# Optimization experiments

Hardware: AMD Instinct MI355X
Metric: run time of the kernel (lower is better)

## Reference

```python
import jax, jax.numpy as jnp
import numpy as np

H = 16          # num_heads (init kwarg)
EPS = 1e-6      # LayerNorm eps


def rope_freqs(L, d):
    # interleaved RoPE freqs, repeat(f, 'i j -> i (j r)', r=2)
    t = jnp.arange(L, dtype=jnp.float32)
    inv = 1.0 / (10000.0 ** (jnp.arange(0, d, 2, dtype=jnp.float32) / d))
    f = t[:, None] * inv[None, :]          # (L, d//2)
    return jnp.repeat(f, 2, axis=-1)       # (L, d)


def rotate_half(x):
    # pair adjacent elems: (x1, x2) -> (-x2, x1)
    shp = x.shape
    x = x.reshape(shp[:-1] + (shp[-1] // 2, 2))
    x1, x2 = x[..., 0], x[..., 1]
    return jnp.stack((-x2, x1), axis=-1).reshape(shp)


def apply_rope(x, f):
    # x: (B, H, L, d), f: (L, d)
    return x * jnp.cos(f) + rotate_half(x) * jnp.sin(f)


def layernorm(x, g, b):
    m = jnp.mean(x, axis=-1, keepdims=True)
    v = jnp.mean(jnp.square(x - m), axis=-1, keepdims=True)
    return (x - m) * jax.lax.rsqrt(v + EPS) * g + b


def setup_inputs() -> dict:
    key = jax.random.key(0)
    ks = jax.random.split(key, 12)
    B, L, D = 2, 2048, 1024
    Dff = 4 * D
    s = 0.02
    inp = {
        'x': jax.random.normal(ks[0], (B, L, D), jnp.float32),
        'ln1_g': jnp.ones((D,), jnp.float32),
        'ln1_b': jnp.zeros((D,), jnp.float32),
        'wq': jax.random.normal(ks[1], (D, D), jnp.float32) * s,
        'bq': jnp.zeros((D,), jnp.float32),
        'wk': jax.random.normal(ks[2], (D, D), jnp.float32) * s,
        'bk': jnp.zeros((D,), jnp.float32),
        'wv': jax.random.normal(ks[3], (D, D), jnp.float32) * s,
        'bv': jnp.zeros((D,), jnp.float32),
        'wo': jax.random.normal(ks[4], (D, D), jnp.float32) * s,
        'bo': jnp.zeros((D,), jnp.float32),
        'ln2_g': jnp.ones((D,), jnp.float32),
        'ln2_b': jnp.zeros((D,), jnp.float32),
        'w1': jax.random.normal(ks[5], (D, Dff), jnp.float32) * s,
        'b1': jnp.zeros((Dff,), jnp.float32),
        'w2': jax.random.normal(ks[6], (Dff, D), jnp.float32) * s,
        'b2': jnp.zeros((D,), jnp.float32),
        # gates are zero-init in the module; use small random so the block is exercised
        'gate_msa': jax.random.normal(ks[7], (1, 1, D), jnp.float32) * 0.1,
        'gate_mlp': jax.random.normal(ks[8], (1, 1, D), jnp.float32) * 0.1,
    }
    return inp


def reference(x, ln1_g, ln1_b, wq, bq, wk, bk, wv, bv, wo, bo,
              ln2_g, ln2_b, w1, b1, w2, b2, gate_msa, gate_mlp):
    B, L, D = x.shape
    hd = D // H
    # --- self-attention branch ---
    h = layernorm(x, ln1_g, ln1_b)
    q = (h @ wq + bq).reshape(B, L, H, hd).transpose(0, 2, 1, 3)  # (B,H,L,hd)
    k = (h @ wk + bk).reshape(B, L, H, hd).transpose(0, 2, 1, 3)
    v = (h @ wv + bv).reshape(B, L, H, hd).transpose(0, 2, 1, 3)
    f = rope_freqs(L, hd)
    q = apply_rope(q, f)
    k = apply_rope(k, f)
    scores = jnp.einsum('bhic,bhjc->bhij', q, k) / np.float32(np.sqrt(hd))
    attn = jax.nn.softmax(scores, axis=-1)  # dropout disabled (eval)
    o = jnp.einsum('bhij,bhjc->bhic', attn, v)
    o = o.transpose(0, 2, 1, 3).reshape(B, L, D)
    x = x + gate_msa * (o @ wo + bo)
    # --- gated MLP branch ---
    h2 = layernorm(x, ln2_g, ln2_b)
    mlp = jax.nn.gelu(h2 @ w1 + b1, approximate=False) @ w2 + b2
    return x + gate_mlp * mlp
```

## Files before the change

kernel.cpp:

```cpp
#include <hip/hip_runtime.h>

typedef unsigned short u16;
typedef __attribute__((ext_vector_type(4))) float f32x4;
typedef __attribute__((ext_vector_type(8))) short bf16x8;

#define DEV static __device__ __forceinline__

DEV float bf2f(u16 u) { unsigned int i = ((unsigned int)u) << 16; return __builtin_bit_cast(float, i); }
DEV u16 f2bf(float f) {
  unsigned int x = __builtin_bit_cast(unsigned int, f);
  x += 0x7fffu + ((x >> 16) & 1u);
  return (u16)(x >> 16);
}

DEV unsigned cvtpk(float lo, float hi) {
  unsigned r;
  asm("v_cvt_pk_bf16_f32 %0, %1, %2" : "=v"(r) : "v"(lo), "v"(hi));
  return r;
}
DEV float exp2a(float x) {
  float r;
  asm("v_exp_f32 %0, %1" : "=v"(r) : "v"(x));
  return r;
}

template <int N>
DEV void wait_vmcnt() {
  if constexpr (N == 0) asm volatile("s_waitcnt vmcnt(0)" ::: "memory");
  else if constexpr (N == 3) asm volatile("s_waitcnt vmcnt(3)" ::: "memory");
  else if constexpr (N == 4) asm volatile("s_waitcnt vmcnt(4)" ::: "memory");
  else static_assert(N == 0, "unsupported vmcnt");
}

DEV void gload16(const u16* g, u16* l) {
  __builtin_amdgcn_global_load_lds(
      (const __attribute__((address_space(1))) unsigned int*)g,
      (__attribute__((address_space(3))) unsigned int*)l, 16, 0, 0);
}

__global__ __launch_bounds__(256) void ln_k(const float* __restrict__ x,
                                            const float* __restrict__ g,
                                            const float* __restrict__ b,
                                            u16* __restrict__ out) {
  const int row = blockIdx.x;
  const int t = threadIdx.x;
  const float4 v = *(const float4*)(x + (size_t)row * 1024 + t * 4);
  float s = v.x + v.y + v.z + v.w;
  float q = v.x * v.x + v.y * v.y + v.z * v.z + v.w * v.w;
#pragma unroll
  for (int m = 1; m < 64; m <<= 1) { s += __shfl_xor(s, m); q += __shfl_xor(q, m); }
  __shared__ float ss[4], qs[4];
  if ((t & 63) == 0) { ss[t >> 6] = s; qs[t >> 6] = q; }
  __syncthreads();
  s = ss[0] + ss[1] + ss[2] + ss[3];
  q = qs[0] + qs[1] + qs[2] + qs[3];
  const float mean = s * (1.0f / 1024.0f);
  const float var = q * (1.0f / 1024.0f) - mean * mean;
  const float rs = rsqrtf(var + 1e-6f);
  const float4 gv = *(const float4*)(g + t * 4);
  const float4 bv = *(const float4*)(b + t * 4);
  ushort4 o;
  o.x = f2bf((v.x - mean) * rs * gv.x + bv.x);
  o.y = f2bf((v.y - mean) * rs * gv.y + bv.y);
  o.z = f2bf((v.z - mean) * rs * gv.z + bv.z);
  o.w = f2bf((v.w - mean) * rs * gv.w + bv.w);
  *(ushort4*)(out + (size_t)row * 1024 + t * 4) = o;
}

__global__ __launch_bounds__(256) void tcvt_k(const float* __restrict__ src,
                                              u16* __restrict__ dst, int K, int N) {
  __shared__ u16 tl[32][33];
  const int k0 = blockIdx.x * 32, n0 = blockIdx.y * 32;
  const int c = threadIdx.x & 31, r0 = threadIdx.x >> 5;
#pragma unroll
  for (int p = 0; p < 4; p++) {
    const int r = p * 8 + r0;
    tl[r][c] = f2bf(src[(size_t)(k0 + r) * N + n0 + c]);
  }
  __syncthreads();
#pragma unroll
  for (int p = 0; p < 4; p++) {
    const int r = p * 8 + r0;
    dst[(size_t)(n0 + r) * K + k0 + c] = tl[c][r];
  }
}

template <int EPI, int TN>
__global__ __launch_bounds__(256) void gemm_bt(const u16* __restrict__ A,
                                               const u16* __restrict__ Bt,
                                               const float* __restrict__ bias,
                                               const float* __restrict__ resid,
                                               const float* __restrict__ gate,
                                               void* __restrict__ outv,
                                               int M, int N, int K) {
  constexpr int MI = (TN == 128) ? 4 : 2;
  constexpr int WRS = (TN == 128) ? 64 : 32;
  constexpr int L = 2 + TN / 64;
  __shared__ __align__(16) u16 lA[3][128 * 32];
  __shared__ __align__(16) u16 lB[3][TN * 32];
  const int tid = threadIdx.x;
  const int lane = tid & 63, wid = tid >> 6;
  const int l4 = lane >> 4, l15 = lane & 15;
  const int wr = (TN == 128) ? (wid >> 1) : wid;
  const int wc = (TN == 128) ? (wid & 1) : 0;
  const int mBase = blockIdx.x * 128;
  const int nBase = blockIdx.y * TN;

  f32x4 acc[MI][4];
#pragma unroll
  for (int i = 0; i < MI; i++)
#pragma unroll
    for (int j = 0; j < 4; j++)
#pragma unroll
      for (int e = 0; e < 4; e++) acc[i][j][e] = 0.f;

  const int sRow = tid >> 2;
  const int sCol = (((tid & 3) ^ ((sRow >> 1) & 3))) * 8;
  const int rsw = (l15 >> 1) & 3;

#define STAGE(bufi, k0)                                                               \
  {                                                                                   \
    _Pragma("unroll") for (int p = 0; p < 2; p++)                                     \
        gload16(A + (size_t)(mBase + p * 64 + sRow) * K + (k0) + sCol,                \
                &lA[bufi][p * 2048 + wid * 512]);                                     \
    _Pragma("unroll") for (int p = 0; p < TN / 64; p++)                               \
        gload16(Bt + (size_t)(nBase + p * 64 + sRow) * K + (k0) + sCol,               \
                &lB[bufi][p * 2048 + wid * 512]);                                     \
  }

  const int nt = K >> 5;
  STAGE(0, 0);
  STAGE(1, 32);
  wait_vmcnt<L>();
  __builtin_amdgcn_s_barrier();
  __builtin_amdgcn_sched_barrier(0);

  int bsel = 0;
  for (int it = 0; it < nt; ++it) {
    bf16x8 af[MI], bfr[4];
#pragma unroll
    for (int mi = 0; mi < MI; mi++)
      af[mi] = *(const bf16x8*)(&lA[bsel][(wr * WRS + mi * 16 + l15) * 32 + (l4 ^ rsw) * 8]);
#pragma unroll
    for (int ni = 0; ni < 4; ni++)
      bfr[ni] = *(const bf16x8*)(&lB[bsel][(wc * 64 + ni * 16 + l15) * 32 + (l4 ^ rsw) * 8]);
    if (it + 2 < nt) {
      int b2 = bsel + 2; if (b2 >= 3) b2 -= 3;
      STAGE(b2, (it + 2) * 32);
    }
#pragma unroll
    for (int mi = 0; mi < MI; mi++)
#pragma unroll
      for (int ni = 0; ni < 4; ni++)
        acc[mi][ni] = __builtin_amdgcn_mfma_f32_16x16x32_bf16(af[mi], bfr[ni], acc[mi][ni], 0, 0, 0);
    if (it + 1 < nt) {
      asm volatile("s_waitcnt lgkmcnt(0)" ::: "memory");
      __builtin_amdgcn_sched_barrier(0);
      if (it + 2 < nt) wait_vmcnt<L>();
      else wait_vmcnt<0>();
      __builtin_amdgcn_s_barrier();
      __builtin_amdgcn_sched_barrier(0);
    }
    bsel = (bsel == 2) ? 0 : bsel + 1;
  }
#undef STAGE

  u16* obf = (u16*)outv;
  float* of = (float*)outv;
#pragma unroll
  for (int mi = 0; mi < MI; mi++) {
#pragma unroll
    for (int ni = 0; ni < 4; ni++) {
      const int row0 = mBase + wr * WRS + mi * 16 + l4 * 4;
      const int col = nBase + wc * 64 + ni * 16 + l15;
      const float bb = bias[col];
#pragma unroll
      for (int r = 0; r < 4; r++) {
        const float v = acc[mi][ni][r] + bb;
        const size_t idx = (size_t)(row0 + r) * N + col;
        if (EPI == 0) {
          obf[idx] = f2bf(v);
        } else if (EPI == 1) {
          const float ge = 0.5f * v * (1.0f + erff(v * 0.70710678118654752f));
          obf[idx] = f2bf(ge);
        } else if (EPI == 2) {
          of[idx] = resid[idx] + gate[col] * v;
        } else {
          of[idx] = of[idx] + gate[col] * v;
        }
      }
    }
  }
}

__global__ __launch_bounds__(256) void rope_k(const u16* __restrict__ qkv,
                                              u16* __restrict__ qr, u16* __restrict__ kr) {
  const int sel = blockIdx.y;
  const int rid = blockIdx.x * 8 + (threadIdx.x >> 5);
  const int i = threadIdx.x & 31;
  const int b = rid >> 15;
  const int h = (rid >> 11) & 15;
  const int t = rid & 2047;
  const u16* src = qkv + (size_t)(b * 2048 + t) * 3072 + sel * 1024 + h * 64 + 2 * i;
  const ushort2 uv = *(const ushort2*)src;
  const float x0 = bf2f(uv.x), x1 = bf2f(uv.y);
  const float inv = __expf(-(float)i * 0.28782313662425572f);
  float sn, cs;
  sincosf((float)t * inv, &sn, &cs);
  const float sc = sel ? 1.0f : 0.18033688011112042f;
  ushort2 ov;
  ov.x = f2bf((x0 * cs - x1 * sn) * sc);
  ov.y = f2bf((x1 * cs + x0 * sn) * sc);
  *(ushort2*)((sel ? kr : qr) + (size_t)rid * 64 + 2 * i) = ov;
}

__global__ __launch_bounds__(256) void vtrans_k(const u16* __restrict__ qkv, u16* __restrict__ vt) {
  __shared__ u16 tl[64][65];
  const int bh = blockIdx.x >> 5;
  const int t0 = (blockIdx.x & 31) * 64;
  const int b = bh >> 4, h = bh & 15;
  const int tid = threadIdx.x;
#pragma unroll
  for (int p = 0; p < 16; p++) {
    const int e = p * 256 + tid;
    const int tr = e >> 6, d = e & 63;
    tl[tr][d] = qkv[(size_t)(b * 2048 + t0 + tr) * 3072 + 2048 + h * 64 + d];
  }
  __syncthreads();
#pragma unroll
  for (int p = 0; p < 16; p++) {
    const int e = p * 256 + tid;
    const int dr = e >> 6, tc = e & 63;
    vt[(size_t)(bh * 64 + dr) * 2048 + t0 + tc] = tl[tc][dr];
  }
}

__global__ __launch_bounds__(256) void attn_k(const u16* __restrict__ q,
                                              const u16* __restrict__ k,
                                              const u16* __restrict__ vt,
                                              u16* __restrict__ o) {
  const int bh = blockIdx.y;
  const int tid = threadIdx.x;
  const int wid = tid >> 6, lane = tid & 63;
  const int l4 = lane >> 4, l15 = lane & 15;
  const int qrow0 = blockIdx.x * 64 + wid * 16;

  __shared__ __align__(16) u16 kls[2][4096];
  __shared__ __align__(16) u16 vls[2][4096];
  __shared__ __align__(16) u16 pls[4][1024];

  const size_t qoff = ((size_t)bh * 2048 + qrow0) * 64;
  const bf16x8 qf0 = *(const bf16x8*)(q + qoff + (size_t)l15 * 64 + l4 * 8);
  const bf16x8 qf1 = *(const bf16x8*)(q + qoff + (size_t)l15 * 64 + 32 + l4 * 8);

  float m0 = -1e30f, ls0 = 0.f;
  f32x4 oacc[4];
#pragma unroll
  for (int ni = 0; ni < 4; ni++)
#pragma unroll
    for (int e = 0; e < 4; e++) oacc[ni][e] = 0.f;

  const char* kg = (const char*)(k + (size_t)bh * 2048 * 64);
  const char* vg = (const char*)(vt + (size_t)bh * 64 * 2048);
  const int sA = tid, sB = 256 + tid;
  const int rA = sA >> 3, cA = ((sA & 7) ^ (rA & 7)) << 4;
  const int rB = sB >> 3, cB = ((sB & 7) ^ (rB & 7)) << 4;
  u16* kd0 = &kls[0][(size_t)(wid * 64) * 8];
  u16* kd1 = &kls[0][(size_t)(256 + wid * 64) * 8];
  u16* vd0 = &vls[0][(size_t)(wid * 64) * 8];
  u16* vd1 = &vls[0][(size_t)(256 + wid * 64) * 8];

#define STAGE(bufi, kv0)                                                            \
  {                                                                                 \
    const int _o = (bufi)*4096;                                                     \
    gload16((const u16*)(kg + (size_t)((kv0) + rA) * 128 + cA), kd0 + _o);          \
    gload16((const u16*)(kg + (size_t)((kv0) + rB) * 128 + cB), kd1 + _o);          \
    gload16((const u16*)(vg + (size_t)rA * 4096 + (kv0)*2 + cA), vd0 + _o);         \
    gload16((const u16*)(vg + (size_t)rB * 4096 + (kv0)*2 + cB), vd1 + _o);         \
  }

  STAGE(0, 0);
  __syncthreads();

  char* P = (char*)pls[wid];
  char* prow0 = P + l15 * 128;
  const int psw = (l15 & 7) << 4;

  int buf = 0;
  for (int it = 0; it < 32; ++it) {
    if (it < 31) STAGE(buf ^ 1, (it + 1) * 64);
    const char* K = (const char*)kls[buf];
    const char* V = (const char*)vls[buf];

    f32x4 s0[4];
#pragma unroll
    for (int kt = 0; kt < 4; kt++) {
      const int row = kt * 16 + l15;
      const int sw = (row & 7) << 4;
      const char* kr = K + row * 128;
      const bf16x8 kf0 = *(const bf16x8*)(kr + ((l4 * 16) ^ sw));
      const bf16x8 kf1 = *(const bf16x8*)(kr + ((64 + l4 * 16) ^ sw));
      f32x4 z0 = {0.f, 0.f, 0.f, 0.f};
      z0 = __builtin_amdgcn_mfma_f32_16x16x32_bf16(kf0, qf0, z0, 0, 0, 0);
      s0[kt] = __builtin_amdgcn_mfma_f32_16x16x32_bf16(kf1, qf1, z0, 0, 0, 0);
    }

    float a00 = fmaxf(fmaxf(s0[0][0], s0[0][1]), fmaxf(s0[0][2], s0[0][3]));
    float a01 = fmaxf(fmaxf(s0[1][0], s0[1][1]), fmaxf(s0[1][2], s0[1][3]));
    float a02 = fmaxf(fmaxf(s0[2][0], s0[2][1]), fmaxf(s0[2][2], s0[2][3]));
    float a03 = fmaxf(fmaxf(s0[3][0], s0[3][1]), fmaxf(s0[3][2], s0[3][3]));
    float pm0 = fmaxf(fmaxf(a00, a01), fmaxf(a02, a03));
    pm0 = fmaxf(pm0, __shfl_xor(pm0, 16));
    pm0 = fmaxf(pm0, __shfl_xor(pm0, 32));
    const bool need = !__all(pm0 <= m0 + 11.54f);
    float al0 = 1.0f;
    if (need) {
      const float mn0 = fmaxf(m0, pm0);
      al0 = exp2a(m0 - mn0);
      m0 = mn0;
    }
#pragma unroll
    for (int kt = 0; kt < 4; kt++)
#pragma unroll
      for (int r = 0; r < 4; r++) s0[kt][r] = exp2a(s0[kt][r] - m0);
    float e00 = (s0[0][0] + s0[0][1]) + (s0[0][2] + s0[0][3]);
    float e01 = (s0[1][0] + s0[1][1]) + (s0[1][2] + s0[1][3]);
    float e02 = (s0[2][0] + s0[2][1]) + (s0[2][2] + s0[2][3]);
    float e03 = (s0[3][0] + s0[3][1]) + (s0[3][2] + s0[3][3]);
    float ps0 = (e00 + e01) + (e02 + e03);
    ps0 += __shfl_xor(ps0, 16);
    ps0 += __shfl_xor(ps0, 32);
    ls0 = ls0 * al0 + ps0;

#pragma unroll
    for (int kt = 0; kt < 4; kt++) {
      uint2 w0;
      w0.x = cvtpk(s0[kt][0], s0[kt][1]);
      w0.y = cvtpk(s0[kt][2], s0[kt][3]);
      *(uint2*)(prow0 + ((kt * 32 + l4 * 8) ^ psw)) = w0;
    }
    asm volatile("s_waitcnt lgkmcnt(0)" ::: "memory");
    const bf16x8 pa0 = *(const bf16x8*)(prow0 + ((l4 * 16) ^ psw));
    const bf16x8 pa1 = *(const bf16x8*)(prow0 + ((64 + l4 * 16) ^ psw));
    if (need) {
      f32x4 av;
#pragma unroll
      for (int r = 0; r < 4; r++) av[r] = __shfl(al0, l4 * 4 + r);
#pragma unroll
      for (int ni = 0; ni < 4; ni++) oacc[ni] *= av;
    }

#pragma unroll
    for (int ni = 0; ni < 4; ni++) {
      const int vrow = ni * 16 + l15;
      const int vsw = (vrow & 7) << 4;
      const char* vr = V + vrow * 128;
      const bf16x8 v0 = *(const bf16x8*)(vr + ((l4 * 16) ^ vsw));
      const bf16x8 v1 = *(const bf16x8*)(vr + ((64 + l4 * 16) ^ vsw));
      oacc[ni] = __builtin_amdgcn_mfma_f32_16x16x32_bf16(pa0, v0, oacc[ni], 0, 0, 0);
      oacc[ni] = __builtin_amdgcn_mfma_f32_16x16x32_bf16(pa1, v1, oacc[ni], 0, 0, 0);
    }
    __syncthreads();
    buf ^= 1;
  }
#undef STAGE

  const float inv0 = 1.0f / ls0;
  f32x4 iv;
#pragma unroll
  for (int r = 0; r < 4; r++) iv[r] = __shfl(inv0, l4 * 4 + r);
  const int b = bh >> 4, h = bh & 15;
#pragma unroll
  for (int r = 0; r < 4; r++) {
    const size_t row = (size_t)b * 2048 + qrow0 + l4 * 4 + r;
#pragma unroll
    for (int ni = 0; ni < 4; ni++)
      o[row * 1024 + h * 64 + ni * 16 + l15] = f2bf(oacc[ni][r] * iv[r]);
  }
}

extern "C" void kernel_launch(void* const* d_in, const int* in_sizes, int n_in,
                              void* d_out, int out_size, void* d_ws, size_t ws_size,
                              hipStream_t stream) {
  (void)in_sizes; (void)n_in; (void)out_size; (void)ws_size;
  const float* x     = (const float*)d_in[0];
  const float* ln1_g = (const float*)d_in[1];
  const float* ln1_b = (const float*)d_in[2];
  const float* wq    = (const float*)d_in[3];
  const float* bq    = (const float*)d_in[4];
  const float* wk    = (const float*)d_in[5];
  const float* bk    = (const float*)d_in[6];
  const float* wv    = (const float*)d_in[7];
  const float* bv    = (const float*)d_in[8];
  const float* wo    = (const float*)d_in[9];
  const float* bo    = (const float*)d_in[10];
  const float* ln2_g = (const float*)d_in[11];
  const float* ln2_b = (const float*)d_in[12];
  const float* w1    = (const float*)d_in[13];
  const float* b1    = (const float*)d_in[14];
  const float* w2    = (const float*)d_in[15];
  const float* b2    = (const float*)d_in[16];
  const float* gmsa  = (const float*)d_in[17];
  const float* gmlp  = (const float*)d_in[18];
  float* out = (float*)d_out;

  char* w = (char*)d_ws;
  auto alloc = [&](size_t bytes) {
    char* p = w;
    w += (bytes + 255) & ~(size_t)255;
    return p;
  };
  u16* h1     = (u16*)alloc(4096UL * 1024 * 2);
  u16* wqkv_t = (u16*)alloc(3072UL * 1024 * 2);
  u16* wo_t   = (u16*)alloc(1024UL * 1024 * 2);
  u16* w1_t   = (u16*)alloc(4096UL * 1024 * 2);
  u16* w2_t   = (u16*)alloc(1024UL * 4096 * 2);
  float* bqkv = (float*)alloc(3072UL * 4);
  u16* qkv    = (u16*)alloc(4096UL * 3072 * 2);
  u16* q_r    = (u16*)alloc(65536UL * 64 * 2);
  u16* k_r    = (u16*)alloc(65536UL * 64 * 2);
  u16* v_t    = (u16*)alloc(65536UL * 64 * 2);
  u16* o_at   = (u16*)alloc(4096UL * 1024 * 2);
  u16* h2     = (u16*)alloc(4096UL * 1024 * 2);
  u16* g1     = (u16*)alloc(4096UL * 4096 * 2);

  tcvt_k<<<dim3(32, 32), 256, 0, stream>>>(wq, wqkv_t, 1024, 1024);
  tcvt_k<<<dim3(32, 32), 256, 0, stream>>>(wk, wqkv_t + 1024 * 1024, 1024, 1024);
  tcvt_k<<<dim3(32, 32), 256, 0, stream>>>(wv, wqkv_t + 2048 * 1024, 1024, 1024);
  tcvt_k<<<dim3(32, 32), 256, 0, stream>>>(wo, wo_t, 1024, 1024);
  tcvt_k<<<dim3(32, 128), 256, 0, stream>>>(w1, w1_t, 1024, 4096);
  tcvt_k<<<dim3(128, 32), 256, 0, stream>>>(w2, w2_t, 4096, 1024);
  hipMemcpyAsync(bqkv,        bq, 1024 * sizeof(float), hipMemcpyDeviceToDevice, stream);
  hipMemcpyAsync(bqkv + 1024, bk, 1024 * sizeof(float), hipMemcpyDeviceToDevice, stream);
  hipMemcpyAsync(bqkv + 2048, bv, 1024 * sizeof(float), hipMemcpyDeviceToDevice, stream);

  ln_k<<<4096, 256, 0, stream>>>(x, ln1_g, ln1_b, h1);
  gemm_bt<0, 128><<<dim3(32, 24), 256, 0, stream>>>(h1, wqkv_t, bqkv, nullptr, nullptr, qkv, 4096, 3072, 1024);
  rope_k<<<dim3(8192, 2), 256, 0, stream>>>(qkv, q_r, k_r);
  vtrans_k<<<1024, 256, 0, stream>>>(qkv, v_t);
  attn_k<<<dim3(32, 32), 256, 0, stream>>>(q_r, k_r, v_t, o_at);
  gemm_bt<2, 64><<<dim3(32, 16), 256, 0, stream>>>(o_at, wo_t, bo, x, gmsa, out, 4096, 1024, 1024);

  ln_k<<<4096, 256, 0, stream>>>(out, ln2_g, ln2_b, h2);
  gemm_bt<1, 128><<<dim3(32, 32), 256, 0, stream>>>(h2, w1_t, b1, nullptr, nullptr, g1, 4096, 4096, 1024);
  gemm_bt<3, 64><<<dim3(32, 16), 256, 0, stream>>>(g1, w2_t, b2, nullptr, gmlp, out, 4096, 1024, 4096);
}
```

Before: 289.1 us.

## Rewrite attention kernel with 32x32x16 MFMA and register-resident P

The flash-attention kernel now gives each wave 32 query rows using 32x32x16 bf16 MFMAs instead of 16x16x32, so each block covers 128 query rows and the grid is halved. The softmax probabilities are packed and exchanged across lane halves with shuffles to form the PV operand directly in registers, which drops the per-iteration LDS round-trip for P. More K/V reuse per staged tile lowers shared-memory and global traffic per unit of work. The cost is higher register pressure (two 16-wide accumulators plus scores) and only 512 blocks, which may reduce occupancy and CU fill.

```diff
diff --git a/kernel.cpp b/kernel.cpp
--- a/kernel.cpp
+++ b/kernel.cpp
@@ -2,6 +2,7 @@
 
 typedef unsigned short u16;
 typedef __attribute__((ext_vector_type(4))) float f32x4;
+typedef __attribute__((ext_vector_type(16))) float f32x16;
 typedef __attribute__((ext_vector_type(8))) short bf16x8;
 
 #define DEV static __device__ __forceinline__
@@ -242,23 +243,22 @@
   const int bh = blockIdx.y;
   const int tid = threadIdx.x;
   const int wid = tid >> 6, lane = tid & 63;
-  const int l4 = lane >> 4, l15 = lane & 15;
-  const int qrow0 = blockIdx.x * 64 + wid * 16;
+  const int h = lane >> 5, rq = lane & 31;
+  const int qrow0 = blockIdx.x * 128 + wid * 32;
 
   __shared__ __align__(16) u16 kls[2][4096];
   __shared__ __align__(16) u16 vls[2][4096];
-  __shared__ __align__(16) u16 pls[4][1024];
-
-  const size_t qoff = ((size_t)bh * 2048 + qrow0) * 64;
-  const bf16x8 qf0 = *(const bf16x8*)(q + qoff + (size_t)l15 * 64 + l4 * 8);
-  const bf16x8 qf1 = *(const bf16x8*)(q + qoff + (size_t)l15 * 64 + 32 + l4 * 8);
+  __shared__ __align__(16) float alds[4][32];
+
+  const u16* qbase = q + ((size_t)bh * 2048 + qrow0 + rq) * 64 + 8 * h;
+  bf16x8 qf[4];
+#pragma unroll
+  for (int db = 0; db < 4; db++) qf[db] = *(const bf16x8*)(qbase + db * 16);
 
   float m0 = -1e30f, ls0 = 0.f;
-  f32x4 oacc[4];
-#pragma unroll
-  for (int ni = 0; ni < 4; ni++)
-#pragma unroll
-    for (int e = 0; e < 4; e++) oacc[ni][e] = 0.f;
+  f32x16 oacc0, oacc1;
+#pragma unroll
+  for (int e = 0; e < 16; e++) { oacc0[e] = 0.f; oacc1[e] = 0.f; }
 
   const char* kg = (const char*)(k + (size_t)bh * 2048 * 64);
   const char* vg = (const char*)(vt + (size_t)bh * 64 * 2048);
@@ -282,9 +282,20 @@
   STAGE(0, 0);
   __syncthreads();
 
-  char* P = (char*)pls[wid];
-  char* prow0 = P + l15 * 128;
-  const int psw = (l15 & 7) << 4;
+  float* AL = alds[wid];
+  const int swz = (rq & 7) << 4;
+
+#define PACK8(S, B, OUT)                                                            \
+  {                                                                                 \
+    unsigned wA = cvtpk(S[B + 0], S[B + 1]), wB_ = cvtpk(S[B + 2], S[B + 3]);       \
+    unsigned wC = cvtpk(S[B + 4], S[B + 5]), wD = cvtpk(S[B + 6], S[B + 7]);        \
+    unsigned xA = __shfl_xor(wA, 32), xB = __shfl_xor(wB_, 32);                     \
+    unsigned xC = __shfl_xor(wC, 32), xD = __shfl_xor(wD, 32);                      \
+    union { unsigned u[4]; bf16x8 v; } _m;                                          \
+    _m.u[0] = h ? xC : wA; _m.u[1] = h ? xD : wB_;                                  \
+    _m.u[2] = h ? wC : xA; _m.u[3] = h ? wD : xB;                                   \
+    OUT = _m.v;                                                                     \
+  }
 
   int buf = 0;
   for (int it = 0; it < 32; ++it) {
@@ -292,90 +303,99 @@
     const char* K = (const char*)kls[buf];
     const char* V = (const char*)vls[buf];
 
-    f32x4 s0[4];
-#pragma unroll
-    for (int kt = 0; kt < 4; kt++) {
-      const int row = kt * 16 + l15;
-      const int sw = (row & 7) << 4;
-      const char* kr = K + row * 128;
-      const bf16x8 kf0 = *(const bf16x8*)(kr + ((l4 * 16) ^ sw));
-      const bf16x8 kf1 = *(const bf16x8*)(kr + ((64 + l4 * 16) ^ sw));
-      f32x4 z0 = {0.f, 0.f, 0.f, 0.f};
-      z0 = __builtin_amdgcn_mfma_f32_16x16x32_bf16(kf0, qf0, z0, 0, 0, 0);
-      s0[kt] = __builtin_amdgcn_mfma_f32_16x16x32_bf16(kf1, qf1, z0, 0, 0, 0);
-    }
-
-    float a00 = fmaxf(fmaxf(s0[0][0], s0[0][1]), fmaxf(s0[0][2], s0[0][3]));
-    float a01 = fmaxf(fmaxf(s0[1][0], s0[1][1]), fmaxf(s0[1][2], s0[1][3]));
-    float a02 = fmaxf(fmaxf(s0[2][0], s0[2][1]), fmaxf(s0[2][2], s0[2][3]));
-    float a03 = fmaxf(fmaxf(s0[3][0], s0[3][1]), fmaxf(s0[3][2], s0[3][3]));
-    float pm0 = fmaxf(fmaxf(a00, a01), fmaxf(a02, a03));
-    pm0 = fmaxf(pm0, __shfl_xor(pm0, 16));
-    pm0 = fmaxf(pm0, __shfl_xor(pm0, 32));
-    const bool need = !__all(pm0 <= m0 + 11.54f);
+    f32x16 st0, st1;
+#pragma unroll
+    for (int e = 0; e < 16; e++) { st0[e] = 0.f; st1[e] = 0.f; }
+#pragma unroll
+    for (int db = 0; db < 4; db++) {
+      const int cb = db * 32;
+      const bf16x8 ka0 = *(const bf16x8*)(K + rq * 128 + ((cb + 16 * h) ^ swz));
+      const bf16x8 ka1 = *(const bf16x8*)(K + (32 + rq) * 128 + ((cb + 16 * h) ^ swz));
+      st0 = __builtin_amdgcn_mfma_f32_32x32x16_bf16(ka0, qf[db], st0, 0, 0, 0);
+      st1 = __builtin_amdgcn_mfma_f32_32x32x16_bf16(ka1, qf[db], st1, 0, 0, 0);
+    }
+
+    float t0 = fmaxf(fmaxf(st0[0], st0[1]), fmaxf(st0[2], st0[3]));
+    float t1 = fmaxf(fmaxf(st0[4], st0[5]), fmaxf(st0[6], st0[7]));
+    float t2 = fmaxf(fmaxf(st0[8], st0[9]), fmaxf(st0[10], st0[11]));
+    float t3 = fmaxf(fmaxf(st0[12], st0[13]), fmaxf(st0[14], st0[15]));
+    float t4 = fmaxf(fmaxf(st1[0], st1[1]), fmaxf(st1[2], st1[3]));
+    float t5 = fmaxf(fmaxf(st1[4], st1[5]), fmaxf(st1[6], st1[7]));
+    float t6 = fmaxf(fmaxf(st1[8], st1[9]), fmaxf(st1[10], st1[11]));
+    float t7 = fmaxf(fmaxf(st1[12], st1[13]), fmaxf(st1[14], st1[15]));
+    float pm = fmaxf(fmaxf(fmaxf(t0, t1), fmaxf(t2, t3)), fmaxf(fmaxf(t4, t5), fmaxf(t6, t7)));
+    pm = fmaxf(pm, __shfl_xor(pm, 32));
+    const bool need = !__all(pm <= m0 + 11.54f);
     float al0 = 1.0f;
     if (need) {
-      const float mn0 = fmaxf(m0, pm0);
-      al0 = exp2a(m0 - mn0);
-      m0 = mn0;
-    }
-#pragma unroll
-    for (int kt = 0; kt < 4; kt++)
-#pragma unroll
-      for (int r = 0; r < 4; r++) s0[kt][r] = exp2a(s0[kt][r] - m0);
-    float e00 = (s0[0][0] + s0[0][1]) + (s0[0][2] + s0[0][3]);
-    float e01 = (s0[1][0] + s0[1][1]) + (s0[1][2] + s0[1][3]);
-    float e02 = (s0[2][0] + s0[2][1]) + (s0[2][2] + s0[2][3]);
-    float e03 = (s0[3][0] + s0[3][1]) + (s0[3][2] + s0[3][3]);
-    float ps0 = (e00 + e01) + (e02 + e03);
-    ps0 += __shfl_xor(ps0, 16);
-    ps0 += __shfl_xor(ps0, 32);
-    ls0 = ls0 * al0 + ps0;
-
-#pragma unroll
-    for (int kt = 0; kt < 4; kt++) {
-      uint2 w0;
-      w0.x = cvtpk(s0[kt][0], s0[kt][1]);
-      w0.y = cvtpk(s0[kt][2], s0[kt][3]);
-      *(uint2*)(prow0 + ((kt * 32 + l4 * 8) ^ psw)) = w0;
-    }
-    asm volatile("s_waitcnt lgkmcnt(0)" ::: "memory");
-    const bf16x8 pa0 = *(const bf16x8*)(prow0 + ((l4 * 16) ^ psw));
-    const bf16x8 pa1 = *(const bf16x8*)(prow0 + ((64 + l4 * 16) ^ psw));
+      const float mn = fmaxf(m0, pm);
+      al0 = exp2a(m0 - mn);
+      m0 = mn;
+    }
+#pragma unroll
+    for (int e = 0; e < 16; e++) {
+      st0[e] = exp2a(st0[e] - m0);
+      st1[e] = exp2a(st1[e] - m0);
+    }
+    float u0 = (st0[0] + st0[1]) + (st0[2] + st0[3]);
+    float u1 = (st0[4] + st0[5]) + (st0[6] + st0[7]);
+    float u2 = (st0[8] + st0[9]) + (st0[10] + st0[11]);
+    float u3 = (st0[12] + st0[13]) + (st0[14] + st0[15]);
+    float u4 = (st1[0] + st1[1]) + (st1[2] + st1[3]);
+    float u5 = (st1[4] + st1[5]) + (st1[6] + st1[7]);
+    float u6 = (st1[8] + st1[9]) + (st1[10] + st1[11]);
+    float u7 = (st1[12] + st1[13]) + (st1[14] + st1[15]);
+    float ps = ((u0 + u1) + (u2 + u3)) + ((u4 + u5) + (u6 + u7));
+    ps += __shfl_xor(ps, 32);
+    ls0 = ls0 * al0 + ps;
+
     if (need) {
-      f32x4 av;
-#pragma unroll
-      for (int r = 0; r < 4; r++) av[r] = __shfl(al0, l4 * 4 + r);
-#pragma unroll
-      for (int ni = 0; ni < 4; ni++) oacc[ni] *= av;
-    }
-
-#pragma unroll
-    for (int ni = 0; ni < 4; ni++) {
-      const int vrow = ni * 16 + l15;
-      const int vsw = (vrow & 7) << 4;
-      const char* vr = V + vrow * 128;
-      const bf16x8 v0 = *(const bf16x8*)(vr + ((l4 * 16) ^ vsw));
-      const bf16x8 v1 = *(const bf16x8*)(vr + ((64 + l4 * 16) ^ vsw));
-      oacc[ni] = __builtin_amdgcn_mfma_f32_16x16x32_bf16(pa0, v0, oacc[ni], 0, 0, 0);
-      oacc[ni] = __builtin_amdgcn_mfma_f32_16x16x32_bf16(pa1, v1, oacc[ni], 0, 0, 0);
+      if (lane < 32) AL[rq] = al0;
+      const f32x4 a0 = *(const f32x4*)((const char*)AL + 16 * h);
+      const f32x4 a1 = *(const f32x4*)((const char*)AL + 32 + 16 * h);
+      const f32x4 a2 = *(const f32x4*)((const char*)AL + 64 + 16 * h);
+      const f32x4 a3 = *(const f32x4*)((const char*)AL + 96 + 16 * h);
+#pragma unroll
+      for (int r = 0; r < 4; r++) {
+        oacc0[r] *= a0[r]; oacc0[4 + r] *= a1[r]; oacc0[8 + r] *= a2[r]; oacc0[12 + r] *= a3[r];
+        oacc1[r] *= a0[r]; oacc1[4 + r] *= a1[r]; oacc1[8 + r] *= a2[r]; oacc1[12 + r] *= a3[r];
+      }
+    }
+
+    bf16x8 pa[4];
+    PACK8(st0, 0, pa[0]);
+    PACK8(st0, 8, pa[1]);
+    PACK8(st1, 0, pa[2]);
+    PACK8(st1, 8, pa[3]);
+
+#pragma unroll
+    for (int kb = 0; kb < 4; kb++) {
+      const int cb = kb * 32;
+      const bf16x8 vb0 = *(const bf16x8*)(V + rq * 128 + ((cb + 16 * h) ^ swz));
+      const bf16x8 vb1 = *(const bf16x8*)(V + (32 + rq) * 128 + ((cb + 16 * h) ^ swz));
+      oacc0 = __builtin_amdgcn_mfma_f32_32x32x16_bf16(pa[kb], vb0, oacc0, 0, 0, 0);
+      oacc1 = __builtin_amdgcn_mfma_f32_32x32x16_bf16(pa[kb], vb1, oacc1, 0, 0, 0);
     }
     __syncthreads();
     buf ^= 1;
   }
 #undef STAGE
-
-  const float inv0 = 1.0f / ls0;
-  f32x4 iv;
-#pragma unroll
-  for (int r = 0; r < 4; r++) iv[r] = __shfl(inv0, l4 * 4 + r);
-  const int b = bh >> 4, h = bh & 15;
-#pragma unroll
-  for (int r = 0; r < 4; r++) {
-    const size_t row = (size_t)b * 2048 + qrow0 + l4 * 4 + r;
-#pragma unroll
-    for (int ni = 0; ni < 4; ni++)
-      o[row * 1024 + h * 64 + ni * 16 + l15] = f2bf(oacc[ni][r] * iv[r]);
+#undef PACK8
+
+  if (lane < 32) AL[rq] = 1.0f / ls0;
+  f32x4 ivg[4];
+  ivg[0] = *(const f32x4*)((const char*)AL + 16 * h);
+  ivg[1] = *(const f32x4*)((const char*)AL + 32 + 16 * h);
+  ivg[2] = *(const f32x4*)((const char*)AL + 64 + 16 * h);
+  ivg[3] = *(const f32x4*)((const char*)AL + 96 + 16 * h);
+  const int b = bh >> 4, hh = bh & 15;
+#pragma unroll
+  for (int r = 0; r < 16; r++) {
+    const int qa = qrow0 + (r & 3) + 8 * (r >> 2) + 4 * h;
+    u16* orow = o + ((size_t)b * 2048 + qa) * 1024 + hh * 64;
+    const float iv = ivg[r >> 2][r & 3];
+    orow[rq] = f2bf(oacc0[r] * iv);
+    orow[32 + rq] = f2bf(oacc1[r] * iv);
   }
 }
 
@@ -438,7 +458,7 @@
   gemm_bt<0, 128><<<dim3(32, 24), 256, 0, stream>>>(h1, wqkv_t, bqkv, nullptr, nullptr, qkv, 4096, 3072, 1024);
   rope_k<<<dim3(8192, 2), 256, 0, stream>>>(qkv, q_r, k_r);
   vtrans_k<<<1024, 256, 0, stream>>>(qkv, v_t);
-  attn_k<<<dim3(32, 32), 256, 0, stream>>>(q_r, k_r, v_t, o_at);
+  attn_k<<<dim3(16, 32), 256, 0, stream>>>(q_r, k_r, v_t, o_at);
   gemm_bt<2, 64><<<dim3(32, 16), 256, 0, stream>>>(o_at, wo_t, bo, x, gmsa, out, 4096, 1024, 1024);
 
   ln_k<<<4096, 256, 0, stream>>>(out, ln2_g, ln2_b, h2);
```

Result: no change. 286.3 us (-1.0%).
